# Optimization experiments

Measured on AMD Instinct MI355X. Metric: run time of the kernel, lower is better.

## Reference

```python
import jax, jax.numpy as jnp
import numpy as np

B, S, D, H = 4, 2048, 1024, 16
DK = D // H  # 64


def setup_inputs() -> dict:
    key = jax.random.key(0)
    ks = jax.random.split(key, 12)
    sc = 0.02
    return {
        "q": jax.random.normal(ks[0], (B, S, D), jnp.float32),
        "k": jax.random.normal(ks[1], (B, S, D), jnp.float32),
        "v": jax.random.normal(ks[2], (B, S, D), jnp.float32),
        "mask": jax.random.randint(ks[3], (B, S, S), 0, 2).astype(bool),
        "Wq": jax.random.normal(ks[4], (H, D, DK), jnp.float32) * sc,
        "bq": jax.random.normal(ks[5], (H, DK), jnp.float32) * sc,
        "Wk": jax.random.normal(ks[6], (H, D, DK), jnp.float32) * sc,
        "bk": jax.random.normal(ks[7], (H, DK), jnp.float32) * sc,
        "Wv": jax.random.normal(ks[8], (H, D, DK), jnp.float32) * sc,
        "bv": jax.random.normal(ks[9], (H, DK), jnp.float32) * sc,
        "Wo": jax.random.normal(ks[10], (D, D), jnp.float32) * sc,
        "bo": jax.random.normal(ks[11], (D,), jnp.float32) * sc,
    }


def reference(q, k, v, mask, Wq, bq, Wk, bk, Wv, bv, Wo, bo):
    # per-head projections, batched over heads: [b,s,d] x [h,d,k] -> [b,h,s,k]
    qh = jnp.einsum('bsd,hdk->bhsk', q, Wq) + bq[None, :, None, :]
    kh = jnp.einsum('bsd,hdk->bhsk', k, Wk) + bk[None, :, None, :]
    vh = jnp.einsum('bsd,hdk->bhsk', v, Wv) + bv[None, :, None, :]
    dk = qh.shape[-1]
    scores = jnp.einsum('bhsk,bhtk->bhst', qh, kh) / (dk ** 0.5)
    # original uses masked_fill(mask == False, -1e-06) -- NOT -inf; keep faithful
    scores = jnp.where(mask[:, None, :, :], scores, jnp.float32(-1e-06))
    attn = jax.nn.softmax(scores, axis=-1)
    out = jnp.einsum('bhst,bhtk->bhsk', attn, vh)
    b, h, s, _ = out.shape
    out = out.transpose(0, 2, 1, 3).reshape(b, s, h * dk)  # concat heads
    return out @ Wo + bo
```

## Files before the change

### kernel.cpp

```cpp
#include <hip/hip_runtime.h>
#include <stdint.h>

#define Bn 4
#define Sn 2048
#define Dn 1024
#define Hn 16
#define DKn 64

typedef __bf16 bf16x8 __attribute__((ext_vector_type(8)));
typedef float f32x4 __attribute__((ext_vector_type(4)));
typedef unsigned short u16;
typedef unsigned long long u64;

union ABFrag { bf16x8 v; uint4 u; };
union V8 { u16 us[8]; uint4 u; };

__device__ __forceinline__ u16 f2bf(float f) {
  union { float f; uint32_t u; } a; a.f = f;
  return (u16)((a.u + 0x7fffu + ((a.u >> 16) & 1u)) >> 16);
}

__device__ __forceinline__ void gload16(const void* g, void* l) {
  __builtin_amdgcn_global_load_lds((const __attribute__((address_space(1))) unsigned int*)g,
                                   (__attribute__((address_space(3))) unsigned int*)l, 16, 0, 0);
}

__device__ __forceinline__ f32x4 zero4() { f32x4 z; z[0]=0.f; z[1]=0.f; z[2]=0.f; z[3]=0.f; return z; }


__global__ void conv_bf16_all(const float* __restrict__ q, const float* __restrict__ k,
                              const float* __restrict__ v, u16* __restrict__ dq,
                              u16* __restrict__ dk, u16* __restrict__ dv) {
  int i = blockIdx.x * 256 + threadIdx.x;
  int seg = i >> 21, j = i & 2097151;
  const float* s = (seg == 0) ? q : (seg == 1) ? k : v;
  u16* d = (seg == 0) ? dq : (seg == 1) ? dk : dv;
  float4 vv = ((const float4*)s)[j];
  V8 o;
  o.us[0] = f2bf(vv.x); o.us[1] = f2bf(vv.y); o.us[2] = f2bf(vv.z); o.us[3] = f2bf(vv.w);
  ((uint2*)d)[j] = make_uint2(o.u.x, o.u.y);
}

__device__ __forceinline__ void tile_tr_body(const float* __restrict__ s, int ss,
                                             u16* __restrict__ d, int ds) {
  __shared__ float t[64 * 65];
  int tid = threadIdx.x;
  int r = tid >> 2, c0 = (tid & 3) * 16;
  #pragma unroll
  for (int j = 0; j < 4; ++j) {
    float4 v = *(const float4*)(s + r * ss + c0 + j * 4);
    t[(c0 + j * 4 + 0) * 65 + r] = v.x;
    t[(c0 + j * 4 + 1) * 65 + r] = v.y;
    t[(c0 + j * 4 + 2) * 65 + r] = v.z;
    t[(c0 + j * 4 + 3) * 65 + r] = v.w;
  }
  __syncthreads();
  V8 o0, o1;
  #pragma unroll
  for (int j = 0; j < 8; ++j) o0.us[j] = f2bf(t[r * 65 + c0 + j]);
  #pragma unroll
  for (int j = 0; j < 8; ++j) o1.us[j] = f2bf(t[r * 65 + c0 + 8 + j]);
  *(uint4*)(d + r * ds + c0) = o0.u;
  *(uint4*)(d + r * ds + c0 + 8) = o1.u;
}

__global__ void prep_w_all(const float* __restrict__ Wq, const float* __restrict__ Wk,
                           const float* __restrict__ Wv, const float* __restrict__ Wo,
                           u16* __restrict__ wcatt, u16* __restrict__ wot) {
  int bid = blockIdx.x;
  if (bid < 768) {
    int w = bid >> 8, h = (bid >> 4) & 15, db = bid & 15;
    const float* src = (w == 0) ? Wq : (w == 1) ? Wk : Wv;
    tile_tr_body(src + (h * 1024 + db * 64) * 64, 64,
                 wcatt + (size_t)(w * 1024 + h * 64) * 1024 + db * 64, 1024);
  } else {
    int b2 = bid - 768;
    int rb = b2 >> 4, cb = b2 & 15;
    tile_tr_body(Wo + (size_t)rb * 64 * 1024 + cb * 64, 1024,
                 wot + (size_t)cb * 64 * 1024 + rb * 64, 1024);
  }
}

__global__ void mask_detect(const uint32_t* __restrict__ mw, int* __restrict__ flag) {
  int t = threadIdx.x;
  uint32_t acc = 0;
  for (int j = 0; j < 4; ++j) acc |= (mw[t * 4 + j] > 1u) ? 1u : 0u;
  unsigned long long bal = __ballot(acc != 0);
  __shared__ int s[4];
  if ((t & 63) == 0) s[t >> 6] = (bal != 0ull) ? 1 : 0;
  __syncthreads();
  if (t == 0) *flag = s[0] | s[1] | s[2] | s[3];
}

__global__ void mask_pack(const void* __restrict__ mraw, const int* __restrict__ flag,
                          u64* __restrict__ mb, int nwords) {
  int i = blockIdx.x * 256 + threadIdx.x;
  if (i >= nwords) return;
  u64 w = 0;
  if (*flag) {
    const uchar4* p = (const uchar4*)mraw + (size_t)i * 16;
    #pragma unroll
    for (int j = 0; j < 16; ++j) {
      uchar4 v = p[j];
      w |= ((u64)(v.x != 0)) << (j * 4 + 0);
      w |= ((u64)(v.y != 0)) << (j * 4 + 1);
      w |= ((u64)(v.z != 0)) << (j * 4 + 2);
      w |= ((u64)(v.w != 0)) << (j * 4 + 3);
    }
  } else {
    const uint4* p = (const uint4*)mraw + (size_t)i * 16;
    #pragma unroll
    for (int j = 0; j < 16; ++j) {
      uint4 v = p[j];
      w |= ((u64)(v.x != 0)) << (j * 4 + 0);
      w |= ((u64)(v.y != 0)) << (j * 4 + 1);
      w |= ((u64)(v.z != 0)) << (j * 4 + 2);
      w |= ((u64)(v.w != 0)) << (j * 4 + 3);
    }
  }
  mb[i] = w;
}

template<int MODE>
__launch_bounds__(256)
__global__ void gemm_kernel(const u16* __restrict__ Aq, const u16* __restrict__ Ak,
                            const u16* __restrict__ Av, const u16* __restrict__ Bm,
                            const float* __restrict__ bq, const float* __restrict__ bk,
                            const float* __restrict__ bv,
                            u16* __restrict__ Oq, u16* __restrict__ Ok, u16* __restrict__ Ov,
                            float* __restrict__ Of) {
  __shared__ char lds[32768];
  char* Al = lds;
  char* Bl = lds + 16384;
  const int tid = threadIdx.x, w = tid >> 6, lane = tid & 63;
  const int n0 = blockIdx.x * 128, m0 = blockIdx.y * 128;
  int which = 0;
  const u16* A = Aq;
  if (MODE == 0) { which = n0 >> 10; A = (which == 0) ? Aq : (which == 1) ? Ak : Av; }

  f32x4 acc[2][8];
  #pragma unroll
  for (int i = 0; i < 2; ++i)
    #pragma unroll
    for (int j = 0; j < 8; ++j) acc[i][j] = zero4();

  for (int kt = 0; kt < 16; ++kt) {
    __syncthreads();
    #pragma unroll
    for (int si = 0; si < 4; ++si) {
      int c = si * 256 + tid, r = c >> 3, cb = c & 7;
      gload16((const char*)A + (((size_t)(m0 + r)) << 11) + (size_t)(kt * 128) + ((cb ^ (r & 7)) << 4),
              Al + si * 4096 + w * 1024);
    }
    #pragma unroll
    for (int si = 0; si < 4; ++si) {
      int c = si * 256 + tid, r = c >> 3, cb = c & 7;
      gload16((const char*)Bm + (((size_t)(n0 + r)) << 11) + (size_t)(kt * 128) + ((cb ^ (r & 7)) << 4),
              Bl + si * 4096 + w * 1024);
    }
    __syncthreads();
    #pragma unroll
    for (int kk = 0; kk < 2; ++kk) {
      ABFrag a0, a1;
      {
        int row = w * 32 + (lane & 15);
        int ch = (lane >> 4) + kk * 4;
        a0.u = *(const uint4*)(Al + row * 128 + ((ch ^ (row & 7)) << 4));
        row += 16;
        a1.u = *(const uint4*)(Al + row * 128 + ((ch ^ (row & 7)) << 4));
      }
      #pragma unroll
      for (int nn = 0; nn < 8; ++nn) {
        int row = nn * 16 + (lane & 15);
        int ch = (lane >> 4) + kk * 4;
        ABFrag bb; bb.u = *(const uint4*)(Bl + row * 128 + ((ch ^ (row & 7)) << 4));
        acc[0][nn] = __builtin_amdgcn_mfma_f32_16x16x32_bf16(a0.v, bb.v, acc[0][nn], 0, 0, 0);
        acc[1][nn] = __builtin_amdgcn_mfma_f32_16x16x32_bf16(a1.v, bb.v, acc[1][nn], 0, 0, 0);
      }
    }
  }

  if (MODE == 0) {
    const float esc = (which == 0) ? 0.18033688011112042f : 1.0f;
    const float* bias = (which == 0) ? bq : (which == 1) ? bk : bv;
    #pragma unroll
    for (int nn = 0; nn < 8; ++nn) {
      int ng = (n0 & 1023) + nn * 16 + (lane & 15);
      int h = ng >> 6, dk = ng & 63;
      float bsv = bias[ng];
      #pragma unroll
      for (int mm = 0; mm < 2; ++mm) {
        #pragma unroll
        for (int r = 0; r < 4; ++r) {
          int mg = m0 + w * 32 + mm * 16 + (lane >> 4) * 4 + r;
          int b = mg >> 11, s = mg & 2047;
          float val = (acc[mm][nn][r] + bsv) * esc;
          if (which == 2) {
            Ov[(((size_t)((b * Hn + h) * DKn + dk)) << 11) + s] = f2bf(val);
          } else {
            u16* O = (which == 0) ? Oq : Ok;
            O[(((size_t)(b * Hn + h)) * Sn + s) * DKn + dk] = f2bf(val);
          }
        }
      }
    }
  } else {
    #pragma unroll
    for (int nn = 0; nn < 8; ++nn) {
      int ng = n0 + nn * 16 + (lane & 15);
      float bsv = bq[ng];
      #pragma unroll
      for (int mm = 0; mm < 2; ++mm) {
        #pragma unroll
        for (int r = 0; r < 4; ++r) {
          int mg = m0 + w * 32 + mm * 16 + (lane >> 4) * 4 + r;
          Of[(size_t)mg * 1024 + ng] = acc[mm][nn][r] + bsv;
        }
      }
    }
  }
}

__launch_bounds__(256, 4)
__global__ void flash_attn(const u16* __restrict__ qh, const u16* __restrict__ kh,
                           const u16* __restrict__ vt, const u64* __restrict__ mb,
                           u16* __restrict__ o) {
  __shared__ char lds[32768];
  char* Klds = lds;
  char* Vlds = lds + 8192;
  const int tid = threadIdx.x, w = tid >> 6, lane = tid & 63;
  const int l15 = lane & 15, g = lane >> 4;
  char* Plds = lds + 16384 + w * 4096;

  int bid = blockIdx.x;
  int wg = (bid & 7) * 128 + (bid >> 3);
  const int bh = wg >> 4, b = bh >> 4, h = bh & 15;
  const int qr = (wg & 15) * 128 + w * 32;

  ABFrag aq[2][2];
  #pragma unroll
  for (int rb = 0; rb < 2; ++rb) {
    const char* qrow = (const char*)(qh + ((size_t)bh * Sn + qr + rb * 16 + l15) * DKn);
    aq[rb][0].u = *(const uint4*)(qrow + g * 16);
    aq[rb][1].u = *(const uint4*)(qrow + 64 + g * 16);
  }

  ABFrag ones;
  {
    unsigned ov = (l15 == 0) ? 0x3F803F80u : 0u;
    ones.u = make_uint4(ov, ov, ov, ov);
  }

  const char* kbase = (const char*)(kh + (size_t)bh * Sn * DKn);
  const char* vbase = (const char*)(vt + (size_t)bh * DKn * Sn);
  const char* mp0 = (const char*)mb + ((size_t)b * Sn + qr + g * 4) * 256;
  const char* mp1 = mp0 + 16 * 256;

  f32x4 oacc[2][4], psacc[2];
  #pragma unroll
  for (int rb = 0; rb < 2; ++rb) {
    #pragma unroll
    for (int nn = 0; nn < 4; ++nn) oacc[rb][nn] = zero4();
    psacc[rb] = zero4();
  }

  const int r0 = tid >> 3, cb0 = tid & 7;
  const int sr = (256 + tid) >> 3, scb = (256 + tid) & 7;
  const int pr_sw = (l15 & 7) << 4;

  for (int t = 0; t < 32; ++t) {
    __syncthreads();
    gload16(kbase + (size_t)(t * 64 + r0) * 128 + ((cb0 ^ (r0 & 7)) << 4), Klds + w * 1024);
    gload16(kbase + (size_t)(t * 64 + sr) * 128 + ((scb ^ (sr & 7)) << 4), Klds + 4096 + w * 1024);
    gload16(vbase + (size_t)r0 * (Sn * 2) + (size_t)(t * 128) + ((cb0 ^ (r0 & 7)) << 4), Vlds + w * 1024);
    gload16(vbase + (size_t)sr * (Sn * 2) + (size_t)(t * 128) + ((scb ^ (sr & 7)) << 4), Vlds + 4096 + w * 1024);
    u64 m0[4], m1[4];
    #pragma unroll
    for (int r = 0; r < 4; ++r) {
      m0[r] = *(const u64*)(mp0 + r * 256 + t * 8);
      m1[r] = *(const u64*)(mp1 + r * 256 + t * 8);
    }
    __syncthreads();

    unsigned lo0[4], hi0[4], lo1[4], hi1[4];
    #pragma unroll
    for (int r = 0; r < 4; ++r) {
      lo0[r] = ((unsigned)m0[r]) >> l15;  hi0[r] = ((unsigned)(m0[r] >> 32)) >> l15;
      lo1[r] = ((unsigned)m1[r]) >> l15;  hi1[r] = ((unsigned)(m1[r] >> 32)) >> l15;
    }

    #pragma unroll
    for (int nn = 0; nn < 4; ++nn) {
      int krow = nn * 16 + l15;
      ABFrag kf0, kf1;
      kf0.u = *(const uint4*)(Klds + krow * 128 + ((g ^ (krow & 7)) << 4));
      kf1.u = *(const uint4*)(Klds + krow * 128 + (((g + 4) ^ (krow & 7)) << 4));
      f32x4 s0 = zero4(), s1 = zero4();
      s0 = __builtin_amdgcn_mfma_f32_16x16x32_bf16(aq[0][0].v, kf0.v, s0, 0, 0, 0);
      s0 = __builtin_amdgcn_mfma_f32_16x16x32_bf16(aq[0][1].v, kf1.v, s0, 0, 0, 0);
      s1 = __builtin_amdgcn_mfma_f32_16x16x32_bf16(aq[1][0].v, kf0.v, s1, 0, 0, 0);
      s1 = __builtin_amdgcn_mfma_f32_16x16x32_bf16(aq[1][1].v, kf1.v, s1, 0, 0, 0);
      unsigned mbit = (nn & 1) ? 0x10000u : 1u;
      #pragma unroll
      for (int r = 0; r < 4; ++r) {
        unsigned w0 = (nn < 2) ? lo0[r] : hi0[r];
        unsigned w1 = (nn < 2) ? lo1[r] : hi1[r];
        float pe0 = __builtin_amdgcn_exp2f(s0[r]);
        float pe1 = __builtin_amdgcn_exp2f(s1[r]);
        float pv0 = (w0 & mbit) ? pe0 : 1.0f;
        float pv1 = (w1 & mbit) ? pe1 : 1.0f;
        int row0 = g * 4 + r;
        int row1 = 16 + g * 4 + r;
        *(__bf16*)(Plds + row0 * 128 + ((nn * 32 + l15 * 2) ^ ((row0 & 7) << 4))) = (__bf16)pv0;
        *(__bf16*)(Plds + row1 * 128 + ((nn * 32 + l15 * 2) ^ ((row1 & 7) << 4))) = (__bf16)pv1;
      }
    }

    __builtin_amdgcn_s_setprio(1);
    #pragma unroll
    for (int kk = 0; kk < 2; ++kk) {
      ABFrag pa0, pa1;
      pa0.u = *(const uint4*)(Plds + l15 * 128 + ((kk * 64 + g * 16) ^ pr_sw));
      pa1.u = *(const uint4*)(Plds + (16 + l15) * 128 + ((kk * 64 + g * 16) ^ pr_sw));
      #pragma unroll
      for (int nn = 0; nn < 4; ++nn) {
        int vrow = nn * 16 + l15;
        ABFrag vb; vb.u = *(const uint4*)(Vlds + vrow * 128 + (((g + kk * 4) ^ (vrow & 7)) << 4));
        oacc[0][nn] = __builtin_amdgcn_mfma_f32_16x16x32_bf16(pa0.v, vb.v, oacc[0][nn], 0, 0, 0);
        oacc[1][nn] = __builtin_amdgcn_mfma_f32_16x16x32_bf16(pa1.v, vb.v, oacc[1][nn], 0, 0, 0);
      }
      psacc[0] = __builtin_amdgcn_mfma_f32_16x16x32_bf16(pa0.v, ones.v, psacc[0], 0, 0, 0);
      psacc[1] = __builtin_amdgcn_mfma_f32_16x16x32_bf16(pa1.v, ones.v, psacc[1], 0, 0, 0);
    }
    __builtin_amdgcn_s_setprio(0);
  }

  #pragma unroll
  for (int rb = 0; rb < 2; ++rb) {
    #pragma unroll
    for (int r = 0; r < 4; ++r) {
      float s = __shfl(psacc[rb][r], lane & 48, 64);
      float inv = 1.f / s;
      int sg = qr + rb * 16 + g * 4 + r;
      #pragma unroll
      for (int nn = 0; nn < 4; ++nn) {
        int col = h * 64 + nn * 16 + l15;
        o[((size_t)(b * Sn) + sg) * Dn + col] = f2bf(oacc[rb][nn][r] * inv);
      }
    }
  }
}


extern "C" void kernel_launch(void* const* d_in, const int* in_sizes, int n_in,
                              void* d_out, int out_size, void* d_ws, size_t ws_size,
                              hipStream_t stream) {
  (void)in_sizes; (void)n_in; (void)out_size; (void)ws_size;
  const float* q  = (const float*)d_in[0];
  const float* k  = (const float*)d_in[1];
  const float* v  = (const float*)d_in[2];
  const void*  mask = d_in[3];
  const float* Wq = (const float*)d_in[4];
  const float* bq = (const float*)d_in[5];
  const float* Wk = (const float*)d_in[6];
  const float* bk = (const float*)d_in[7];
  const float* Wv = (const float*)d_in[8];
  const float* bv = (const float*)d_in[9];
  const float* Wo = (const float*)d_in[10];
  const float* bo = (const float*)d_in[11];
  float* out = (float*)d_out;

  char* ws = (char*)d_ws;
  const size_t SZ = (size_t)8192 * 1024 * 2;
  u16* qbf   = (u16*)(ws);
  u16* kbf   = (u16*)(ws + SZ);
  u16* vbf   = (u16*)(ws + 2 * SZ);
  u16* Wcatt = (u16*)(ws + 3 * SZ);
  u16* Wot   = (u16*)(ws + 3 * SZ + 6291456);
  u16* qhp   = (u16*)(ws + 3 * SZ + 8388608);
  u16* khp   = (u16*)((char*)qhp + SZ);
  u16* vtp   = (u16*)((char*)khp + SZ);
  int* flag  = (int*)((char*)vtp + SZ);

  conv_bf16_all<<<24576, 256, 0, stream>>>(q, k, v, qbf, kbf, vbf);
  prep_w_all<<<1024, 256, 0, stream>>>(Wq, Wk, Wv, Wo, Wcatt, Wot);

  gemm_kernel<0><<<dim3(24, 64), 256, 0, stream>>>(qbf, kbf, vbf, Wcatt, bq, bk, bv,
                                                   qhp, khp, vtp, nullptr);

  mask_detect<<<1, 256, 0, stream>>>((const uint32_t*)mask, flag);
  u64* mbw = (u64*)vbf;
  mask_pack<<<1024, 256, 0, stream>>>(mask, flag, mbw, 262144);

  u16* oc = qbf;
  flash_attn<<<1024, 256, 0, stream>>>(qhp, khp, vtp, mbw, oc);

  gemm_kernel<1><<<dim3(8, 64), 256, 0, stream>>>(oc, nullptr, nullptr, Wot, bo,
                                                  nullptr, nullptr, nullptr,
                                                  nullptr, nullptr, out);
}
```

Measured before the change: 440.5 us.

## Enlarge flash-attention tiles to 64 query rows per wave and swizzle GEMM blocks

Each wave in the attention kernel now handles 64 query rows instead of 32, so every K/V tile loaded into LDS is reused across twice as many rows. The grid is halved and the P buffer in LDS is doubled. The QK MFMA operands are swapped so each lane holds one query row and stores four probabilities at once as packed bf16. This cuts per-lane mask loads and the scattered 2-byte LDS stores, and the GEMM grid gets a block-ID swizzle for L2 locality. The cost is more registers, lower occupancy (launch bounds 2) and fewer blocks to fill the CUs.

```diff
diff --git a/kernel.cpp b/kernel.cpp
--- a/kernel.cpp
+++ b/kernel.cpp
@@ -14,6 +14,7 @@
 
 union ABFrag { bf16x8 v; uint4 u; };
 union V8 { u16 us[8]; uint4 u; };
+union PK4 { u16 us[4]; uint2 u2; };
 
 __device__ __forceinline__ u16 f2bf(float f) {
   union { float f; uint32_t u; } a; a.f = f;
@@ -133,7 +134,11 @@
   char* Al = lds;
   char* Bl = lds + 16384;
   const int tid = threadIdx.x, w = tid >> 6, lane = tid & 63;
-  const int n0 = blockIdx.x * 128, m0 = blockIdx.y * 128;
+  const int NBX = (MODE == 0) ? 24 : 8;
+  int wid = blockIdx.y * NBX + blockIdx.x;
+  int tot = NBX * 64;
+  int swz = (wid & 7) * (tot >> 3) + (wid >> 3);
+  const int n0 = (swz % NBX) * 128, m0 = (swz / NBX) * 128;
   int which = 0;
   const u16* A = Aq;
   if (MODE == 0) { which = n0 >> 10; A = (which == 0) ? Aq : (which == 1) ? Ak : Av; }
@@ -221,25 +226,25 @@
   }
 }
 
-__launch_bounds__(256, 4)
+__launch_bounds__(256, 2)
 __global__ void flash_attn(const u16* __restrict__ qh, const u16* __restrict__ kh,
                            const u16* __restrict__ vt, const u64* __restrict__ mb,
                            u16* __restrict__ o) {
-  __shared__ char lds[32768];
+  __shared__ char lds[49152];
   char* Klds = lds;
   char* Vlds = lds + 8192;
   const int tid = threadIdx.x, w = tid >> 6, lane = tid & 63;
   const int l15 = lane & 15, g = lane >> 4;
-  char* Plds = lds + 16384 + w * 4096;
+  char* Plds = lds + 16384 + w * 8192;
 
   int bid = blockIdx.x;
-  int wg = (bid & 7) * 128 + (bid >> 3);
-  const int bh = wg >> 4, b = bh >> 4, h = bh & 15;
-  const int qr = (wg & 15) * 128 + w * 32;
-
-  ABFrag aq[2][2];
-  #pragma unroll
-  for (int rb = 0; rb < 2; ++rb) {
+  int wg = (bid & 7) * 64 + (bid >> 3);
+  const int bh = wg >> 3, b = bh >> 4, h = bh & 15;
+  const int qr = (wg & 7) * 256 + w * 64;
+
+  ABFrag aq[4][2];
+  #pragma unroll
+  for (int rb = 0; rb < 4; ++rb) {
     const char* qrow = (const char*)(qh + ((size_t)bh * Sn + qr + rb * 16 + l15) * DKn);
     aq[rb][0].u = *(const uint4*)(qrow + g * 16);
     aq[rb][1].u = *(const uint4*)(qrow + 64 + g * 16);
@@ -253,12 +258,11 @@
 
   const char* kbase = (const char*)(kh + (size_t)bh * Sn * DKn);
   const char* vbase = (const char*)(vt + (size_t)bh * DKn * Sn);
-  const char* mp0 = (const char*)mb + ((size_t)b * Sn + qr + g * 4) * 256;
-  const char* mp1 = mp0 + 16 * 256;
-
-  f32x4 oacc[2][4], psacc[2];
-  #pragma unroll
-  for (int rb = 0; rb < 2; ++rb) {
+  const char* mpl = (const char*)mb + ((size_t)b * Sn + qr + l15) * 256;
+
+  f32x4 oacc[4][4], psacc[4];
+  #pragma unroll
+  for (int rb = 0; rb < 4; ++rb) {
     #pragma unroll
     for (int nn = 0; nn < 4; ++nn) oacc[rb][nn] = zero4();
     psacc[rb] = zero4();
@@ -266,7 +270,6 @@
 
   const int r0 = tid >> 3, cb0 = tid & 7;
   const int sr = (256 + tid) >> 3, scb = (256 + tid) & 7;
-  const int pr_sw = (l15 & 7) << 4;
 
   for (int t = 0; t < 32; ++t) {
     __syncthreads();
@@ -274,20 +277,10 @@
     gload16(kbase + (size_t)(t * 64 + sr) * 128 + ((scb ^ (sr & 7)) << 4), Klds + 4096 + w * 1024);
     gload16(vbase + (size_t)r0 * (Sn * 2) + (size_t)(t * 128) + ((cb0 ^ (r0 & 7)) << 4), Vlds + w * 1024);
     gload16(vbase + (size_t)sr * (Sn * 2) + (size_t)(t * 128) + ((scb ^ (sr & 7)) << 4), Vlds + 4096 + w * 1024);
-    u64 m0[4], m1[4];
-    #pragma unroll
-    for (int r = 0; r < 4; ++r) {
-      m0[r] = *(const u64*)(mp0 + r * 256 + t * 8);
-      m1[r] = *(const u64*)(mp1 + r * 256 + t * 8);
-    }
+    u64 mw[4];
+    #pragma unroll
+    for (int rb = 0; rb < 4; ++rb) mw[rb] = *(const u64*)(mpl + rb * 4096 + t * 8);
     __syncthreads();
-
-    unsigned lo0[4], hi0[4], lo1[4], hi1[4];
-    #pragma unroll
-    for (int r = 0; r < 4; ++r) {
-      lo0[r] = ((unsigned)m0[r]) >> l15;  hi0[r] = ((unsigned)(m0[r] >> 32)) >> l15;
-      lo1[r] = ((unsigned)m1[r]) >> l15;  hi1[r] = ((unsigned)(m1[r] >> 32)) >> l15;
-    }
 
     #pragma unroll
     for (int nn = 0; nn < 4; ++nn) {
@@ -295,48 +288,52 @@
       ABFrag kf0, kf1;
       kf0.u = *(const uint4*)(Klds + krow * 128 + ((g ^ (krow & 7)) << 4));
       kf1.u = *(const uint4*)(Klds + krow * 128 + (((g + 4) ^ (krow & 7)) << 4));
-      f32x4 s0 = zero4(), s1 = zero4();
-      s0 = __builtin_amdgcn_mfma_f32_16x16x32_bf16(aq[0][0].v, kf0.v, s0, 0, 0, 0);
-      s0 = __builtin_amdgcn_mfma_f32_16x16x32_bf16(aq[0][1].v, kf1.v, s0, 0, 0, 0);
-      s1 = __builtin_amdgcn_mfma_f32_16x16x32_bf16(aq[1][0].v, kf0.v, s1, 0, 0, 0);
-      s1 = __builtin_amdgcn_mfma_f32_16x16x32_bf16(aq[1][1].v, kf1.v, s1, 0, 0, 0);
-      unsigned mbit = (nn & 1) ? 0x10000u : 1u;
-      #pragma unroll
-      for (int r = 0; r < 4; ++r) {
-        unsigned w0 = (nn < 2) ? lo0[r] : hi0[r];
-        unsigned w1 = (nn < 2) ? lo1[r] : hi1[r];
-        float pe0 = __builtin_amdgcn_exp2f(s0[r]);
-        float pe1 = __builtin_amdgcn_exp2f(s1[r]);
-        float pv0 = (w0 & mbit) ? pe0 : 1.0f;
-        float pv1 = (w1 & mbit) ? pe1 : 1.0f;
-        int row0 = g * 4 + r;
-        int row1 = 16 + g * 4 + r;
-        *(__bf16*)(Plds + row0 * 128 + ((nn * 32 + l15 * 2) ^ ((row0 & 7) << 4))) = (__bf16)pv0;
-        *(__bf16*)(Plds + row1 * 128 + ((nn * 32 + l15 * 2) ^ ((row1 & 7) << 4))) = (__bf16)pv1;
+      #pragma unroll
+      for (int rb = 0; rb < 4; ++rb) {
+        f32x4 s = zero4();
+        s = __builtin_amdgcn_mfma_f32_16x16x32_bf16(kf0.v, aq[rb][0].v, s, 0, 0, 0);
+        s = __builtin_amdgcn_mfma_f32_16x16x32_bf16(kf1.v, aq[rb][1].v, s, 0, 0, 0);
+        u64 wsh = mw[rb] >> (g * 4);
+        unsigned wsel = (nn < 2) ? (unsigned)wsh : (unsigned)(wsh >> 32);
+        unsigned bit0 = (nn & 1) ? 0x10000u : 1u;
+        PK4 pk;
+        #pragma unroll
+        for (int r = 0; r < 4; ++r) {
+          float pe = __builtin_amdgcn_exp2f(s[r]);
+          float pv = (wsel & (bit0 << r)) ? pe : 1.0f;
+          pk.us[r] = f2bf(pv);
+        }
+        int row = rb * 16 + l15;
+        *(uint2*)(Plds + row * 128 + ((nn * 32 + g * 8) ^ ((row & 7) << 4))) = pk.u2;
       }
     }
 
     __builtin_amdgcn_s_setprio(1);
     #pragma unroll
     for (int kk = 0; kk < 2; ++kk) {
-      ABFrag pa0, pa1;
-      pa0.u = *(const uint4*)(Plds + l15 * 128 + ((kk * 64 + g * 16) ^ pr_sw));
-      pa1.u = *(const uint4*)(Plds + (16 + l15) * 128 + ((kk * 64 + g * 16) ^ pr_sw));
+      ABFrag pa[4];
+      #pragma unroll
+      for (int rb = 0; rb < 4; ++rb) {
+        int prow = rb * 16 + l15;
+        pa[rb].u = *(const uint4*)(Plds + prow * 128 + ((kk * 64 + g * 16) ^ ((prow & 7) << 4)));
+      }
       #pragma unroll
       for (int nn = 0; nn < 4; ++nn) {
         int vrow = nn * 16 + l15;
         ABFrag vb; vb.u = *(const uint4*)(Vlds + vrow * 128 + (((g + kk * 4) ^ (vrow & 7)) << 4));
-        oacc[0][nn] = __builtin_amdgcn_mfma_f32_16x16x32_bf16(pa0.v, vb.v, oacc[0][nn], 0, 0, 0);
-        oacc[1][nn] = __builtin_amdgcn_mfma_f32_16x16x32_bf16(pa1.v, vb.v, oacc[1][nn], 0, 0, 0);
-      }
-      psacc[0] = __builtin_amdgcn_mfma_f32_16x16x32_bf16(pa0.v, ones.v, psacc[0], 0, 0, 0);
-      psacc[1] = __builtin_amdgcn_mfma_f32_16x16x32_bf16(pa1.v, ones.v, psacc[1], 0, 0, 0);
+        #pragma unroll
+        for (int rb = 0; rb < 4; ++rb)
+          oacc[rb][nn] = __builtin_amdgcn_mfma_f32_16x16x32_bf16(pa[rb].v, vb.v, oacc[rb][nn], 0, 0, 0);
+      }
+      #pragma unroll
+      for (int rb = 0; rb < 4; ++rb)
+        psacc[rb] = __builtin_amdgcn_mfma_f32_16x16x32_bf16(pa[rb].v, ones.v, psacc[rb], 0, 0, 0);
     }
     __builtin_amdgcn_s_setprio(0);
   }
 
   #pragma unroll
-  for (int rb = 0; rb < 2; ++rb) {
+  for (int rb = 0; rb < 4; ++rb) {
     #pragma unroll
     for (int r = 0; r < 4; ++r) {
       float s = __shfl(psacc[rb][r], lane & 48, 64);
@@ -393,7 +390,7 @@
   mask_pack<<<1024, 256, 0, stream>>>(mask, flag, mbw, 262144);
 
   u16* oc = qbf;
-  flash_attn<<<1024, 256, 0, stream>>>(qhp, khp, vtp, mbw, oc);
+  flash_attn<<<512, 256, 0, stream>>>(qhp, khp, vtp, mbw, oc);
 
   gemm_kernel<1><<<dim3(8, 64), 256, 0, stream>>>(oc, nullptr, nullptr, Wot, bo,
                                                   nullptr, nullptr, nullptr,
```

Result: no change. 448.4 us (+1.8%).
